# Kernel optimization log

Measured on AMD Instinct MI355X. Metric: run time of the kernel, lower is better.

Reference implementation:

```python
import jax, jax.numpy as jnp
import numpy as np
import math

B, T, C = 1, 2048, 2048
N_HEAD = 32
N_QUERY_GROUPS = 8
HEAD_SIZE = 64
ROPE_N_ELEM = 16  # int(0.25 * 64)
Q_PER_KV = N_HEAD // N_QUERY_GROUPS  # 4
QKV_DIM = (N_HEAD + 2 * N_QUERY_GROUPS) * HEAD_SIZE  # 3072


def setup_inputs() -> dict:
    key = jax.random.key(0)
    ks = jax.random.split(key, 7)
    x = jax.random.normal(ks[0], (B, T, C), dtype=jnp.float32)
    # realistic rope tables
    inv_freq = 1.0 / (10000.0 ** (jnp.arange(0, ROPE_N_ELEM, 2, dtype=jnp.float32) / ROPE_N_ELEM))
    t = jnp.arange(T, dtype=jnp.float32)
    freqs = jnp.outer(t, inv_freq)                       # [T, rope/2]
    emb = jnp.concatenate([freqs, freqs], axis=-1)       # [T, rope]
    cos, sin = jnp.cos(emb), jnp.sin(emb)
    s = 0.02
    W_attn = jax.random.normal(ks[1], (QKV_DIM, C), dtype=jnp.float32) * s
    b_attn = jax.random.normal(ks[2], (QKV_DIM,), dtype=jnp.float32) * s
    W_proj = jax.random.normal(ks[3], (C, N_HEAD * HEAD_SIZE), dtype=jnp.float32) * s
    b_proj = jax.random.normal(ks[4], (C,), dtype=jnp.float32) * s
    return {"x": x, "cos": cos, "sin": sin, "W_attn": W_attn, "b_attn": b_attn,
            "W_proj": W_proj, "b_proj": b_proj}


def _apply_rope(t, cos, sin):
    # t: [B, H, T, rope]; cos/sin: [T, rope]
    half = t.shape[-1] // 2
    t1, t2 = t[..., :half], t[..., half:]
    rotated = jnp.concatenate([-t2, t1], axis=-1)
    return t * cos + rotated * sin


def reference(x, cos, sin, W_attn, b_attn, W_proj, b_proj):
    Bc, Tc, Cc = x.shape
    qkv = x @ W_attn.T + b_attn                                   # [B, T, 3072]
    qkv = qkv.reshape(Bc, Tc, N_QUERY_GROUPS, Q_PER_KV + 2, HEAD_SIZE)
    qkv = qkv.transpose(0, 2, 3, 1, 4)                            # [B, G, q_per_kv+2, T, hs]
    q = qkv[:, :, :Q_PER_KV]                                      # [B, G, q_per_kv, T, hs]
    k = qkv[:, :, Q_PER_KV:Q_PER_KV + 1]                          # [B, G, 1, T, hs]
    v = qkv[:, :, Q_PER_KV + 1:]
    # GQA expand (n_query_groups != n_head, prefill path)
    k = jnp.broadcast_to(k, (Bc, N_QUERY_GROUPS, Q_PER_KV, Tc, HEAD_SIZE))
    v = jnp.broadcast_to(v, (Bc, N_QUERY_GROUPS, Q_PER_KV, Tc, HEAD_SIZE))
    q = q.reshape(Bc, N_HEAD, Tc, HEAD_SIZE)
    k = k.reshape(Bc, N_HEAD, Tc, HEAD_SIZE)
    v = v.reshape(Bc, N_HEAD, Tc, HEAD_SIZE)
    # partial RoPE on first ROPE_N_ELEM dims
    q = jnp.concatenate([_apply_rope(q[..., :ROPE_N_ELEM], cos, sin), q[..., ROPE_N_ELEM:]], axis=-1)
    k = jnp.concatenate([_apply_rope(k[..., :ROPE_N_ELEM], cos, sin), k[..., ROPE_N_ELEM:]], axis=-1)
    # causal SDPA with scale 1/sqrt(head_size)
    scale = 1.0 / math.sqrt(HEAD_SIZE)
    scores = jnp.einsum('bhqd,bhkd->bhqk', q, k) * scale          # [B, H, T, T]
    causal = jnp.tril(jnp.ones((Tc, Tc), dtype=bool))
    scores = jnp.where(causal, scores, jnp.finfo(scores.dtype).min)
    attn = jax.nn.softmax(scores, axis=-1)
    y = jnp.einsum('bhqk,bhkd->bhqd', attn, v)                    # [B, H, T, hs]
    y = y.transpose(0, 2, 1, 3).reshape(Bc, Tc, N_HEAD * HEAD_SIZE)
    return y @ W_proj.T + b_proj
```

## Files before the change

### kernel.cpp

```cpp
#include <hip/hip_runtime.h>
#include <hip/hip_bf16.h>

using u16 = unsigned short;
typedef float f32x4 __attribute__((ext_vector_type(4)));
typedef __bf16 bf16x8 __attribute__((ext_vector_type(8)));

#define T_SEQ 2048
#define C_DIM 2048
#define QKV_DIM 3072
#define N_HEAD 32
#define N_GROUPS 8
#define HEAD_SIZE 64
#define ROPE_N 16
#define NEG_BIG (-1e30f)
#define LS 72

__device__ inline float bf2f(u16 u) {
    union { float f; unsigned v; } x; x.v = ((unsigned)u) << 16; return x.f;
}
__device__ inline u16 f2bf(float f) {
    __bf16 h = (__bf16)f;
    return *(u16*)&h;
}
__device__ inline int4 cvt8(int4 lo, int4 hi) {
    const float* fa = (const float*)&lo;
    const float* fb = (const float*)&hi;
    __attribute__((aligned(16))) u16 o[8] = {
        f2bf(fa[0]), f2bf(fa[1]), f2bf(fa[2]), f2bf(fa[3]),
        f2bf(fb[0]), f2bf(fb[1]), f2bf(fb[2]), f2bf(fb[3]) };
    return *(const int4*)o;
}

__device__ __forceinline__ int detect_fp32(const unsigned* __restrict__ xw) {
    int cnt = 0;
#pragma unroll
    for (int i = 0; i < 128; i++) {
        unsigned w = xw[i];
        cnt += (((w >> 7)  & 0xFF) >= 0xC0);
        cnt += (((w >> 23) & 0xFF) >= 0xC0);
    }
    return cnt > 8;
}

__device__ __forceinline__ void gl_lds16(const u16* g, u16* l) {
    __builtin_amdgcn_global_load_lds(
        (const __attribute__((address_space(1))) unsigned int*)g,
        (__attribute__((address_space(3))) unsigned int*)l,
        16, 0, 0);
}

struct ConvDesc {
    const void* src[7];
    u16*        dst[7];
    int         off8[8];
};

__global__ void convert_all(ConvDesc cd)
{
    const int fl = detect_fp32((const unsigned*)cd.src[0]);
    int gid = blockIdx.x * blockDim.x + threadIdx.x;
    if (gid >= cd.off8[7]) return;
    int seg = 0;
#pragma unroll
    for (int s = 1; s < 7; s++) seg += (gid >= cd.off8[s]);
    int i = (gid - cd.off8[seg]) * 8;
    if (fl) {
        const float4* s = (const float4*)((const float*)cd.src[seg] + i);
        *(int4*)(cd.dst[seg] + i) = cvt8(*(const int4*)&s[0], *(const int4*)&s[1]);
    } else {
        *(int4*)(cd.dst[seg] + i) = *(const int4*)((const u16*)cd.src[seg] + i);
    }
}

__global__ __launch_bounds__(256) void gemm_qkv_rope(
    const u16* __restrict__ A, const u16* __restrict__ W,
    const u16* __restrict__ bias,
    const u16* __restrict__ ccos, const u16* __restrict__ csin,
    u16* __restrict__ Qout, u16* __restrict__ Kout, u16* __restrict__ Vtout)
{
    __shared__ __attribute__((aligned(16))) u16 lds_a[128 * 32];
    __shared__ __attribute__((aligned(16))) u16 lds_b[128 * 32];

    const int tid  = threadIdx.x;
    const int wave = tid >> 6;
    const int lane = tid & 63;
    const int quad = lane >> 4;
    const int l16  = lane & 15;
    const int wr = wave >> 1, wc = wave & 1;
    const int bm = blockIdx.y * 128;
    const int bn = blockIdx.x * 128;
    const int K = C_DIM;

    f32x4 acc[4][4] = {};

    const int s0 = tid, s1 = tid + 256;
    const int r0 = s0 >> 2, c0 = (s0 & 3) * 8;
    const int r1 = s1 >> 2, c1 = (s1 & 3) * 8;

    for (int k0 = 0; k0 < K; k0 += 32) {
        __syncthreads();
        gl_lds16(A + (size_t)(bm + r0) * K + k0 + c0, lds_a + s0 * 8);
        gl_lds16(A + (size_t)(bm + r1) * K + k0 + c1, lds_a + s1 * 8);
        gl_lds16(W + (size_t)(bn + r0) * K + k0 + c0, lds_b + s0 * 8);
        gl_lds16(W + (size_t)(bn + r1) * K + k0 + c1, lds_b + s1 * 8);
        __syncthreads();

        bf16x8 afr[4], bfr[4];
#pragma unroll
        for (int i = 0; i < 4; i++)
            afr[i] = *(const bf16x8*)(lds_a + (wr * 64 + i * 16 + l16) * 32 + quad * 8);
#pragma unroll
        for (int j = 0; j < 4; j++)
            bfr[j] = *(const bf16x8*)(lds_b + (wc * 64 + j * 16 + l16) * 32 + quad * 8);
#pragma unroll
        for (int i = 0; i < 4; i++)
#pragma unroll
            for (int j = 0; j < 4; j++)
                acc[i][j] = __builtin_amdgcn_mfma_f32_16x16x32_bf16(afr[i], bfr[j], acc[i][j], 0, 0, 0);
    }

#pragma unroll
    for (int j = 0; j < 4; j++) {
        const int colb = bn + wc * 64 + j * 16;
        const int col  = colb + l16;
        const int slot = (colb % 384) >> 6;
        const int g    = colb / 384;
        const int dbase = colb & 63;
        const int d    = dbase + l16;
        const float bv = bf2f(bias[col]);
        const bool rope = (dbase == 0) && (slot != 5);
#pragma unroll
        for (int i = 0; i < 4; i++) {
            const int trow = bm + wr * 64 + i * 16 + quad * 4;
#pragma unroll
            for (int r = 0; r < 4; r++) {
                float v = acc[i][j][r] + bv;
                float outv = v;
                if (rope) {
                    float part = __shfl_xor(v, 8, 64);
                    float rot = (l16 < 8) ? -part : part;
                    float cc = bf2f(ccos[(trow + r) * ROPE_N + l16]);
                    float ss = bf2f(csin[(trow + r) * ROPE_N + l16]);
                    outv = v * cc + rot * ss;
                }
                const int t = trow + r;
                if (slot < 4) {
                    int hh = g * 4 + slot;
                    Qout[((size_t)hh * T_SEQ + t) * 64 + d] = f2bf(outv * 0.125f);
                } else if (slot == 4) {
                    Kout[((size_t)g * T_SEQ + t) * 64 + d] = f2bf(outv);
                } else {
                    Vtout[((size_t)g * 64 + d) * T_SEQ + t] = f2bf(outv);
                }
            }
        }
    }
}

__global__ __launch_bounds__(256) void gemm_bt(
    const u16* __restrict__ A, const u16* __restrict__ W,
    const u16* __restrict__ bias, u16* __restrict__ Cout,
    int M, int N, int K, const unsigned* __restrict__ xprobe)
{
    __shared__ __attribute__((aligned(16))) u16 lds_a[64 * 32];
    __shared__ __attribute__((aligned(16))) u16 lds_b[128 * 32];

    const int tid  = threadIdx.x;
    const int wave = tid >> 6;
    const int lane = tid & 63;
    const int quad = lane >> 4;
    const int l16  = lane & 15;
    const int bm = blockIdx.y * 64;
    const int bn = blockIdx.x * 128;
    const int fl = detect_fp32(xprobe);

    f32x4 acc[4][2] = {};

    const int ra = tid >> 2, ca = (tid & 3) * 8;
    const int rb1 = (tid + 256) >> 2;

    for (int k0 = 0; k0 < K; k0 += 32) {
        __syncthreads();
        gl_lds16(A + (size_t)(bm + ra) * K + k0 + ca,  lds_a + tid * 8);
        gl_lds16(W + (size_t)(bn + ra) * K + k0 + ca,  lds_b + tid * 8);
        gl_lds16(W + (size_t)(bn + rb1) * K + k0 + ca, lds_b + (tid + 256) * 8);
        __syncthreads();

        bf16x8 afr[4], bfr[2];
#pragma unroll
        for (int i = 0; i < 4; i++)
            afr[i] = *(const bf16x8*)(lds_a + (i * 16 + l16) * 32 + quad * 8);
#pragma unroll
        for (int j = 0; j < 2; j++)
            bfr[j] = *(const bf16x8*)(lds_b + (wave * 32 + j * 16 + l16) * 32 + quad * 8);
#pragma unroll
        for (int i = 0; i < 4; i++)
#pragma unroll
            for (int j = 0; j < 2; j++)
                acc[i][j] = __builtin_amdgcn_mfma_f32_16x16x32_bf16(afr[i], bfr[j], acc[i][j], 0, 0, 0);
    }

#pragma unroll
    for (int i = 0; i < 4; i++) {
        int row = bm + i * 16 + quad * 4;
#pragma unroll
        for (int j = 0; j < 2; j++) {
            int col = bn + wave * 32 + j * 16 + l16;
            float bv = bf2f(bias[col]);
#pragma unroll
            for (int r = 0; r < 4; r++) {
                float v = acc[i][j][r] + bv;
                size_t idx = (size_t)(row + r) * N + col;
                if (fl) ((float*)Cout)[idx] = v;
                else    Cout[idx] = f2bf(v);
            }
        }
    }
}

__global__ __launch_bounds__(256) void flash_attn(
    const u16* __restrict__ Q, const u16* __restrict__ K,
    const u16* __restrict__ Vt, u16* __restrict__ Y)
{
    __shared__ __attribute__((aligned(16))) u16 lds_q[64 * LS];
    __shared__ __attribute__((aligned(16))) u16 lds_k[2][64 * LS];
    __shared__ __attribute__((aligned(16))) u16 lds_vt[2][64 * LS];
    __shared__ __attribute__((aligned(16))) u16 lds_p[4][16 * LS];

    const int h  = blockIdx.y;
    const int g  = h >> 2;
    const int tid  = threadIdx.x;
    const int wave = tid >> 6;
    const int lane = tid & 63;
    const int quad = lane >> 4;
    const int l16  = lane & 15;
    const int NQT = T_SEQ / 64;

    const u16* Qh = Q  + (size_t)h * T_SEQ * 64;
    const u16* Kg = K  + (size_t)g * T_SEQ * 64;
    const u16* Vg = Vt + (size_t)g * 64 * T_SEQ;

    const int srow = tid >> 3, scc = (tid & 7) * 8;

    int4 kr0, kr1, vr0, vr1;
    auto load_tile = [&](int k0) {
        kr0 = *(const int4*)(Kg + (size_t)(k0 + srow) * 64 + scc);
        kr1 = *(const int4*)(Kg + (size_t)(k0 + srow + 32) * 64 + scc);
        vr0 = *(const int4*)(Vg + (size_t)srow * T_SEQ + k0 + scc);
        vr1 = *(const int4*)(Vg + (size_t)(srow + 32) * T_SEQ + k0 + scc);
    };

    for (int pass = 0; pass < 2; pass++) {
        const int qt = pass ? (NQT - 1 - blockIdx.x) : blockIdx.x;
        const int q0 = qt * 64;

        __syncthreads();
        for (int s = tid; s < 512; s += 256) {
            int row = s >> 3, cc = (s & 7) * 8;
            *(int4*)(lds_q + row * LS + cc) =
                *(const int4*)(Qh + (size_t)(q0 + row) * 64 + cc);
        }
        __syncthreads();

        bf16x8 a_q[2];
#pragma unroll
        for (int ks = 0; ks < 2; ks++)
            a_q[ks] = *(const bf16x8*)(lds_q + (wave * 16 + l16) * LS + ks * 32 + quad * 8);

        float rs[4] = {0.f, 0.f, 0.f, 0.f};
        f32x4 o_acc[4] = {};

        load_tile(0);

        for (int kt = 0; kt <= qt; kt++) {
            const int p = kt & 1;
            *(int4*)(lds_k[p]  + srow * LS + scc)        = kr0;
            *(int4*)(lds_k[p]  + (srow + 32) * LS + scc) = kr1;
            *(int4*)(lds_vt[p] + srow * LS + scc)        = vr0;
            *(int4*)(lds_vt[p] + (srow + 32) * LS + scc) = vr1;
            __syncthreads();
            if (kt < qt) load_tile((kt + 1) * 64);

            f32x4 sc[4] = {};
#pragma unroll
            for (int ks = 0; ks < 2; ks++)
#pragma unroll
                for (int t = 0; t < 4; t++) {
                    bf16x8 bk = *(const bf16x8*)(lds_k[p] + (t * 16 + l16) * LS + ks * 32 + quad * 8);
                    sc[t] = __builtin_amdgcn_mfma_f32_16x16x32_bf16(a_q[ks], bk, sc[t], 0, 0, 0);
                }

            if (kt == qt) {
                const int row_g = q0 + wave * 16 + quad * 4;
                const int k0 = kt * 64;
#pragma unroll
                for (int t = 0; t < 4; t++) {
                    int col_g = k0 + t * 16 + l16;
#pragma unroll
                    for (int r = 0; r < 4; r++)
                        if (col_g > row_g + r) sc[t][r] = NEG_BIG;
                }
            }

#pragma unroll
            for (int t = 0; t < 4; t++) {
                int colo = t * 16 + l16;
#pragma unroll
                for (int r = 0; r < 4; r++) {
                    float pv = __expf(sc[t][r]);
                    rs[r] += pv;
                    lds_p[wave][(quad * 4 + r) * LS + colo] = f2bf(pv);
                }
            }

#pragma unroll
            for (int ks = 0; ks < 2; ks++) {
                bf16x8 apf = *(const bf16x8*)(lds_p[wave] + l16 * LS + ks * 32 + quad * 8);
#pragma unroll
                for (int t = 0; t < 4; t++) {
                    bf16x8 bvf = *(const bf16x8*)(lds_vt[p] + (t * 16 + l16) * LS + ks * 32 + quad * 8);
                    o_acc[t] = __builtin_amdgcn_mfma_f32_16x16x32_bf16(apf, bvf, o_acc[t], 0, 0, 0);
                }
            }
        }

#pragma unroll
        for (int off = 1; off < 16; off <<= 1)
#pragma unroll
            for (int r = 0; r < 4; r++)
                rs[r] += __shfl_xor(rs[r], off, 64);

#pragma unroll
        for (int t = 0; t < 4; t++)
#pragma unroll
            for (int r = 0; r < 4; r++) {
                int row = q0 + wave * 16 + quad * 4 + r;
                int d   = t * 16 + l16;
                Y[(size_t)row * (N_HEAD * HEAD_SIZE) + h * 64 + d] = f2bf(o_acc[t][r] / rs[r]);
            }
    }
}

extern "C" void kernel_launch(void* const* d_in, const int* in_sizes, int n_in,
                              void* d_out, int out_size, void* d_ws, size_t ws_size,
                              hipStream_t stream)
{
    u16* base = (u16*)d_ws;

    u16* cx   = base;
    u16* cWa  = cx  + (size_t)T_SEQ * C_DIM;
    u16* cba  = cWa + (size_t)QKV_DIM * C_DIM;
    u16* cWp  = cba + QKV_DIM;
    u16* cbp  = cWp + (size_t)C_DIM * C_DIM;
    u16* ccos = cbp + C_DIM;
    u16* csin = ccos + (size_t)T_SEQ * ROPE_N;
    u16* Qb   = csin + (size_t)T_SEQ * ROPE_N;
    u16* Kb   = Qb + (size_t)N_HEAD * T_SEQ * HEAD_SIZE;
    u16* Vtb  = Kb + (size_t)N_GROUPS * T_SEQ * HEAD_SIZE;
    u16* Yb   = Vtb + (size_t)N_GROUPS * T_SEQ * HEAD_SIZE;

    dim3 blk(256);

    ConvDesc cd;
    const int sizes[7] = { T_SEQ * C_DIM, T_SEQ * ROPE_N, T_SEQ * ROPE_N,
                           QKV_DIM * C_DIM, QKV_DIM, C_DIM * C_DIM, C_DIM };
    u16* dsts[7] = { cx, ccos, csin, cWa, cba, cWp, cbp };
    int acc8 = 0;
    for (int i = 0; i < 7; i++) {
        cd.src[i] = d_in[i];
        cd.dst[i] = dsts[i];
        cd.off8[i] = acc8;
        acc8 += sizes[i] / 8;
    }
    cd.off8[7] = acc8;
    convert_all<<<dim3((acc8 + 255) / 256), blk, 0, stream>>>(cd);

    gemm_qkv_rope<<<dim3(QKV_DIM / 128, T_SEQ / 128), blk, 0, stream>>>(
        cx, cWa, cba, ccos, csin, Qb, Kb, Vtb);
    flash_attn<<<dim3(T_SEQ / 128, N_HEAD), blk, 0, stream>>>(Qb, Kb, Vtb, Yb);
    gemm_bt<<<dim3(C_DIM / 128, T_SEQ / 64), blk, 0, stream>>>(
        Yb, cWp, cbp, (u16*)d_out, T_SEQ, C_DIM, N_HEAD * HEAD_SIZE,
        (const unsigned*)d_in[0]);
}
```

Before: 272.1 us.

## Double-buffer GEMM LDS tiles with K=64 steps and XOR-swizzled layout

```diff
diff --git a/kernel.cpp b/kernel.cpp
--- a/kernel.cpp
+++ b/kernel.cpp
@@ -78,8 +78,8 @@
     const u16* __restrict__ ccos, const u16* __restrict__ csin,
     u16* __restrict__ Qout, u16* __restrict__ Kout, u16* __restrict__ Vtout)
 {
-    __shared__ __attribute__((aligned(16))) u16 lds_a[128 * 32];
-    __shared__ __attribute__((aligned(16))) u16 lds_b[128 * 32];
+    __shared__ __attribute__((aligned(16))) u16 lds_a[2][128 * 64];
+    __shared__ __attribute__((aligned(16))) u16 lds_b[2][128 * 64];
 
     const int tid  = threadIdx.x;
     const int wave = tid >> 6;
@@ -93,30 +93,47 @@
 
     f32x4 acc[4][4] = {};
 
-    const int s0 = tid, s1 = tid + 256;
-    const int r0 = s0 >> 2, c0 = (s0 & 3) * 8;
-    const int r1 = s1 >> 2, c1 = (s1 & 3) * 8;
-
-    for (int k0 = 0; k0 < K; k0 += 32) {
+    int srow[4], sgc[4];
+#pragma unroll
+    for (int k = 0; k < 4; k++) {
+        int s = tid + k * 256;
+        srow[k] = s >> 3;
+        sgc[k]  = (s & 7) ^ (srow[k] & 7);
+    }
+    const int xh = l16 & 7;
+
+    auto stage = [&](int k0, int p) {
+#pragma unroll
+        for (int k = 0; k < 4; k++) {
+            int s = tid + k * 256;
+            gl_lds16(A + (size_t)(bm + srow[k]) * K + k0 + sgc[k] * 8, lds_a[p] + s * 8);
+            gl_lds16(W + (size_t)(bn + srow[k]) * K + k0 + sgc[k] * 8, lds_b[p] + s * 8);
+        }
+    };
+
+    stage(0, 0);
+    const int nsteps = K / 64;
+    for (int kt = 0; kt < nsteps; kt++) {
+        const int p = kt & 1;
         __syncthreads();
-        gl_lds16(A + (size_t)(bm + r0) * K + k0 + c0, lds_a + s0 * 8);
-        gl_lds16(A + (size_t)(bm + r1) * K + k0 + c1, lds_a + s1 * 8);
-        gl_lds16(W + (size_t)(bn + r0) * K + k0 + c0, lds_b + s0 * 8);
-        gl_lds16(W + (size_t)(bn + r1) * K + k0 + c1, lds_b + s1 * 8);
-        __syncthreads();
-
-        bf16x8 afr[4], bfr[4];
+        if (kt + 1 < nsteps) stage((kt + 1) * 64, p ^ 1);
+
+        bf16x8 afr[4][2], bfr[4][2];
 #pragma unroll
         for (int i = 0; i < 4; i++)
-            afr[i] = *(const bf16x8*)(lds_a + (wr * 64 + i * 16 + l16) * 32 + quad * 8);
-#pragma unroll
-        for (int j = 0; j < 4; j++)
-            bfr[j] = *(const bf16x8*)(lds_b + (wc * 64 + j * 16 + l16) * 32 + quad * 8);
-#pragma unroll
-        for (int i = 0; i < 4; i++)
-#pragma unroll
-            for (int j = 0; j < 4; j++)
-                acc[i][j] = __builtin_amdgcn_mfma_f32_16x16x32_bf16(afr[i], bfr[j], acc[i][j], 0, 0, 0);
+#pragma unroll
+            for (int ks = 0; ks < 2; ks++) {
+                int c = (ks * 4 + quad) ^ xh;
+                afr[i][ks] = *(const bf16x8*)(lds_a[p] + (wr * 64 + i * 16 + l16) * 64 + c * 8);
+                bfr[i][ks] = *(const bf16x8*)(lds_b[p] + (wc * 64 + i * 16 + l16) * 64 + c * 8);
+            }
+#pragma unroll
+        for (int ks = 0; ks < 2; ks++)
+#pragma unroll
+            for (int i = 0; i < 4; i++)
+#pragma unroll
+                for (int j = 0; j < 4; j++)
+                    acc[i][j] = __builtin_amdgcn_mfma_f32_16x16x32_bf16(afr[i][ks], bfr[j][ks], acc[i][j], 0, 0, 0);
     }
 
 #pragma unroll
@@ -162,8 +179,8 @@
     const u16* __restrict__ bias, u16* __restrict__ Cout,
     int M, int N, int K, const unsigned* __restrict__ xprobe)
 {
-    __shared__ __attribute__((aligned(16))) u16 lds_a[64 * 32];
-    __shared__ __attribute__((aligned(16))) u16 lds_b[128 * 32];
+    __shared__ __attribute__((aligned(16))) u16 lds_a[2][64 * 64];
+    __shared__ __attribute__((aligned(16))) u16 lds_b[2][128 * 64];
 
     const int tid  = threadIdx.x;
     const int wave = tid >> 6;
@@ -176,28 +193,53 @@
 
     f32x4 acc[4][2] = {};
 
-    const int ra = tid >> 2, ca = (tid & 3) * 8;
-    const int rb1 = (tid + 256) >> 2;
-
-    for (int k0 = 0; k0 < K; k0 += 32) {
+    int srow[4], sgc[4];
+#pragma unroll
+    for (int k = 0; k < 4; k++) {
+        int s = tid + k * 256;
+        srow[k] = s >> 3;
+        sgc[k]  = (s & 7) ^ (srow[k] & 7);
+    }
+    const int xh = l16 & 7;
+
+    auto stage = [&](int k0, int p) {
+#pragma unroll
+        for (int k = 0; k < 2; k++) {
+            int s = tid + k * 256;
+            gl_lds16(A + (size_t)(bm + srow[k]) * K + k0 + sgc[k] * 8, lds_a[p] + s * 8);
+        }
+#pragma unroll
+        for (int k = 0; k < 4; k++) {
+            int s = tid + k * 256;
+            gl_lds16(W + (size_t)(bn + srow[k]) * K + k0 + sgc[k] * 8, lds_b[p] + s * 8);
+        }
+    };
+
+    stage(0, 0);
+    const int nsteps = K / 64;
+    for (int kt = 0; kt < nsteps; kt++) {
+        const int p = kt & 1;
         __syncthreads();
-        gl_lds16(A + (size_t)(bm + ra) * K + k0 + ca,  lds_a + tid * 8);
-        gl_lds16(W + (size_t)(bn + ra) * K + k0 + ca,  lds_b + tid * 8);
-        gl_lds16(W + (size_t)(bn + rb1) * K + k0 + ca, lds_b + (tid + 256) * 8);
-        __syncthreads();
-
-        bf16x8 afr[4], bfr[2];
-#pragma unroll
-        for (int i = 0; i < 4; i++)
-            afr[i] = *(const bf16x8*)(lds_a + (i * 16 + l16) * 32 + quad * 8);
-#pragma unroll
-        for (int j = 0; j < 2; j++)
-            bfr[j] = *(const bf16x8*)(lds_b + (wave * 32 + j * 16 + l16) * 32 + quad * 8);
-#pragma unroll
-        for (int i = 0; i < 4; i++)
+        if (kt + 1 < nsteps) stage((kt + 1) * 64, p ^ 1);
+
+        bf16x8 afr[4][2], bfr[2][2];
+#pragma unroll
+        for (int ks = 0; ks < 2; ks++) {
+            int c = ((ks * 4 + quad) ^ xh) * 8;
+#pragma unroll
+            for (int i = 0; i < 4; i++)
+                afr[i][ks] = *(const bf16x8*)(lds_a[p] + (i * 16 + l16) * 64 + c);
 #pragma unroll
             for (int j = 0; j < 2; j++)
-                acc[i][j] = __builtin_amdgcn_mfma_f32_16x16x32_bf16(afr[i], bfr[j], acc[i][j], 0, 0, 0);
+                bfr[j][ks] = *(const bf16x8*)(lds_b[p] + (wave * 32 + j * 16 + l16) * 64 + c);
+        }
+#pragma unroll
+        for (int ks = 0; ks < 2; ks++)
+#pragma unroll
+            for (int i = 0; i < 4; i++)
+#pragma unroll
+                for (int j = 0; j < 2; j++)
+                    acc[i][j] = __builtin_amdgcn_mfma_f32_16x16x32_bf16(afr[i][ks], bfr[j][ks], acc[i][j], 0, 0, 0);
     }
 
 #pragma unroll
```

New measurement: 261.1 us. 1.04x faster.
